# Kernel optimization log

Measured on AMD Instinct MI355X. Metric: run time of the kernel, lower is better.

## Reference

```python
import jax, jax.numpy as jnp
import numpy as np

H = 8        # num_heads
KNN = 16     # k nearest neighbors
D = 256      # input_dim
LN_EPS = 1e-5


def _make_params(key, D):
    ks = jax.random.split(key, 10)
    def lin(k, din, dout):
        k1, k2 = jax.random.split(k)
        lim = 1.0 / np.sqrt(din)
        W = jax.random.uniform(k1, (din, dout), jnp.float32, -lim, lim)
        b = jax.random.uniform(k2, (dout,), jnp.float32, -lim, lim)
        return W, b
    Wq, bq = lin(ks[0], D, D)
    Wk, bk = lin(ks[1], D, D)
    Wv, bv = lin(ks[2], D, D)
    Wo1, bo1 = lin(ks[3], D, D)
    ln_g = jnp.ones((D,), jnp.float32)
    ln_b = jnp.zeros((D,), jnp.float32)
    Wo2, bo2 = lin(ks[4], D, D)
    return dict(Wq=Wq, bq=bq, Wk=Wk, bk=bk, Wv=Wv, bv=bv,
                Wo1=Wo1, bo1=bo1, ln_g=ln_g, ln_b=ln_b, Wo2=Wo2, bo2=bo2)


def setup_inputs() -> dict:
    key = jax.random.key(0)
    k1, k2, k3, k4, k5 = jax.random.split(key, 5)
    B, N, M = 2, 2048, 4096
    inp = {
        "src": jax.random.normal(k1, (B, N, 3), jnp.float32),
        "tgt": jax.random.normal(k2, (B, M, 3), jnp.float32),
        "src_fea": jax.random.normal(k3, (B, N, D), jnp.float32),
        "tgt_fea": jax.random.normal(k4, (B, M, D), jnp.float32),
    }
    inp.update(_make_params(k5, D))
    return inp


def _cdist(x, y):
    # Euclidean distance [B,N,M], matching torch.cdist(p=2)
    x2 = jnp.sum(x * x, axis=-1, keepdims=True)          # [B,N,1]
    y2 = jnp.sum(y * y, axis=-1, keepdims=True)          # [B,M,1]
    sq = x2 + jnp.swapaxes(y2, -1, -2) - 2.0 * jnp.einsum('bnc,bmc->bnm', x, y)
    return jnp.sqrt(jnp.maximum(sq, 0.0))


def _layernorm(x, g, b):
    mu = jnp.mean(x, axis=-1, keepdims=True)
    var = jnp.mean((x - mu) ** 2, axis=-1, keepdims=True)
    return (x - mu) * jax.lax.rsqrt(var + LN_EPS) * g + b


def reference(src, tgt, src_fea, tgt_fea, Wq, bq, Wk, bk, Wv, bv,
              Wo1, bo1, ln_g, ln_b, Wo2, bo2):
    B, N, Dm = src_fea.shape
    M = tgt.shape[1]
    dk = Dm // H
    scale = dk ** (-0.5)

    # kNN mask: distances [B,N,M], topk smallest -> boolean mask
    dist = _cdist(src, tgt)
    _, knn_idx = jax.lax.top_k(-dist, KNN)               # [B,N,KNN]
    bi = jnp.arange(B)[:, None, None]
    ni = jnp.arange(N)[None, :, None]
    mask = jnp.zeros((B, N, M), bool).at[bi, ni, knn_idx].set(True)

    # projections -> [B,H,*,dk]
    Q = (src_fea @ Wq + bq).reshape(B, N, H, dk).transpose(0, 2, 1, 3)
    K = (tgt_fea @ Wk + bk).reshape(B, M, H, dk).transpose(0, 2, 1, 3)
    V = (tgt_fea @ Wv + bv).reshape(B, M, H, dk).transpose(0, 2, 1, 3)

    scores = jnp.einsum('bhnd,bhmd->bhnm', Q, K) * scale
    scores = jnp.where(mask[:, None], scores, -jnp.inf)
    attn = jax.nn.softmax(scores, axis=-1)               # [B,H,N,M]

    out = jnp.einsum('bhnm,bhmd->bhnd', attn, V)
    out = out.transpose(0, 2, 1, 3).reshape(B, N, Dm)

    x = out + src_fea
    h = jax.nn.relu(_layernorm(x @ Wo1 + bo1, ln_g, ln_b))
    updated = h @ Wo2 + bo2

    avg_attn = jnp.mean(attn, axis=1)                    # [B,N,M]
    return updated, avg_attn
```

## Files before the change

kernel.cpp:

```cpp
#include <hip/hip_runtime.h>
#include <math.h>

#define BB 2
#define NN 2048
#define MM 4096
#define DD 256
#define HH 8
#define DK 32
#define KNN 16

typedef __attribute__((ext_vector_type(8))) short short8;
typedef __attribute__((ext_vector_type(4))) short short4v;
typedef __attribute__((ext_vector_type(4))) float f32x4;
typedef unsigned long long u64;
typedef unsigned short u16;

static __device__ __forceinline__ u16 f2bf(float f) {
    union { float f; unsigned u; } v; v.f = f;
    unsigned r = v.u + 0x7FFF + ((v.u >> 16) & 1);
    return (u16)(r >> 16);
}
static __device__ __forceinline__ float bf2f(u16 u) {
    union { unsigned u; float f; } v; v.u = ((unsigned)u) << 16;
    return v.f;
}

__global__ __launch_bounds__(256)
void wtrans(const float* W0, const float* W1, const float* W2, const float* W3, const float* W4,
            u16* O0, u16* O1, u16* O2, u16* O3, u16* O4)
{
    __shared__ float tile[64][65];
    const int bid = blockIdx.x;
    const int m = bid >> 4, tl = bid & 15;
    const int tr = (tl >> 2) * 64, tc = (tl & 3) * 64;
    const float* W = m == 0 ? W0 : m == 1 ? W1 : m == 2 ? W2 : m == 3 ? W3 : W4;
    u16*        O = m == 0 ? O0 : m == 1 ? O1 : m == 2 ? O2 : m == 3 ? O3 : O4;
    const int c = threadIdx.x & 63, r4 = threadIdx.x >> 6;
    #pragma unroll
    for (int i = 0; i < 16; ++i) {
        const int r = (r4 << 4) + i;
        tile[r][c] = W[(size_t)(tr + r) * 256 + tc + c];
    }
    __syncthreads();
    #pragma unroll
    for (int i = 0; i < 16; ++i) {
        const int cc = (r4 << 4) + i;
        O[(size_t)(tc + cc) * 256 + tr + c] = f2bf(tile[c][cc]);
    }
}

static __device__ __forceinline__ void gemm64_body(
    const float* __restrict__ A, size_t row0, const u16* __restrict__ WT, int col0,
    u16* As, u16* Bs, int t, f32x4 acc[2][2])
{
    const int lane = t & 63, w = t >> 6;
    const int wr = (w >> 1) * 32, wc = (w & 1) * 32;
    for (int k0 = 0; k0 < 256; k0 += 64) {
        #pragma unroll
        for (int e = 0; e < 2; ++e) {
            const int flat = t + (e << 8);
            const int r = flat >> 3, kc = (flat & 7) << 3;
            const int off = ((r << 7) + (kc << 1)) ^ ((r & 7) << 4);
            const float* ap = A + (row0 + r) * 256 + k0 + kc;
            float4 a0 = *(const float4*)ap;
            float4 a1 = *(const float4*)(ap + 4);
            short8 s;
            s[0] = (short)f2bf(a0.x); s[1] = (short)f2bf(a0.y);
            s[2] = (short)f2bf(a0.z); s[3] = (short)f2bf(a0.w);
            s[4] = (short)f2bf(a1.x); s[5] = (short)f2bf(a1.y);
            s[6] = (short)f2bf(a1.z); s[7] = (short)f2bf(a1.w);
            *(short8*)((char*)As + off) = s;
            *(short8*)((char*)Bs + off) = *(const short8*)(WT + (size_t)(col0 + r) * 256 + k0 + kc);
        }
        __syncthreads();
        #pragma unroll
        for (int kk = 0; kk < 64; kk += 32) {
            const int kbo = (kk + ((lane >> 4) << 3)) << 1;
            short8 af[2], bfr[2];
            #pragma unroll
            for (int i = 0; i < 2; ++i) {
                const int ra = wr + (i << 4) + (lane & 15);
                af[i]  = *(const short8*)((const char*)As + (((ra << 7) + kbo) ^ ((ra & 7) << 4)));
                const int rb = wc + (i << 4) + (lane & 15);
                bfr[i] = *(const short8*)((const char*)Bs + (((rb << 7) + kbo) ^ ((rb & 7) << 4)));
            }
            #pragma unroll
            for (int mi = 0; mi < 2; ++mi)
                #pragma unroll
                for (int ni = 0; ni < 2; ++ni)
                    acc[mi][ni] = __builtin_amdgcn_mfma_f32_16x16x32_bf16(af[mi], bfr[ni], acc[mi][ni], 0, 0, 0);
        }
        __syncthreads();
    }
}

__global__ __launch_bounds__(256, 4)
void mega_kernel(const float* __restrict__ src, const float* __restrict__ tgt,
                 int* __restrict__ knn_idx,
                 const float* __restrict__ tgt_fea, const float* __restrict__ src_fea,
                 const u16* __restrict__ WTq, const u16* __restrict__ WTkv,
                 const float* __restrict__ bq, const float* __restrict__ bk,
                 const float* __restrict__ bv,
                 float* __restrict__ Qb, u16* __restrict__ Kbf, u16* __restrict__ Vbf,
                 float* __restrict__ avg)
{
    __shared__ u16 As[64 * 64];
    __shared__ u16 Bs[64 * 64];
    const int bid = blockIdx.x;
    const int t = threadIdx.x;
    const int lane = t & 63;
    const int lid = bid / 11;
    const int role = bid % 11;

    if (role < 4) {
        const int kb = lid * 4 + role;
        const int bn = (kb << 2) + (t >> 6);
        const int b = bn >> 11;
        const float* sp = src + (size_t)bn * 3;
        const float px = sp[0], py = sp[1], pz = sp[2];
        const float x2 = px * px + py * py + pz * pz;
        const float* tb = tgt + (size_t)b * MM * 3;
        unsigned key[64];
        #pragma unroll
        for (int j = 0; j < 64; ++j) {
            const int m = (j << 6) + lane;
            const float tx = tb[m * 3 + 0], ty = tb[m * 3 + 1], tz = tb[m * 3 + 2];
            const float y2 = tx * tx + ty * ty + tz * tz;
            const float dt = px * tx + py * ty + pz * tz;
            float d = (x2 + y2) - 2.0f * dt;
            d = d > 0.f ? d : 0.f;
            const unsigned q20 = (unsigned)fminf(d * 32768.0f, 1048575.0f);
            key[j] = (q20 << 12) | (unsigned)m;
        }
        unsigned last1 = 0;
        unsigned mykey = 0xFFFFFFFFu;
        for (int sel = 0; sel < 20; ++sel) {
            unsigned c0 = ~0u, c1 = ~0u, c2 = ~0u, c3 = ~0u;
            #pragma unroll
            for (int j = 0; j < 64; j += 4) {
                const unsigned u0 = key[j + 0] - last1; c0 = u0 < c0 ? u0 : c0;
                const unsigned u1 = key[j + 1] - last1; c1 = u1 < c1 ? u1 : c1;
                const unsigned u2 = key[j + 2] - last1; c2 = u2 < c2 ? u2 : c2;
                const unsigned u3 = key[j + 3] - last1; c3 = u3 < c3 ? u3 : c3;
            }
            unsigned best = c0 < c1 ? c0 : c1;
            const unsigned bst2 = c2 < c3 ? c2 : c3;
            best = best < bst2 ? best : bst2;
            #pragma unroll
            for (int s2 = 32; s2; s2 >>= 1) {
                const unsigned o = __shfl_xor(best, s2, 64);
                best = o < best ? o : best;
            }
            const unsigned winner = best + last1;
            if (lane == sel) mykey = winner;
            last1 = winner + 1;
        }
        const int midx = (int)(mykey & 0xFFFu);
        u64 ex = ~0ULL;
        if (lane < 20) {
            const float* tp = tb + (size_t)midx * 3;
            const double pxd = px, pyd = py, pzd = pz;
            const double tx = tp[0], ty = tp[1], tz = tp[2];
            const double x2d = pxd * pxd + pyd * pyd + pzd * pzd;
            const double y2d = tx * tx + ty * ty + tz * tz;
            const double dtd = pxd * tx + pyd * ty + pzd * tz;
            double dd = (x2d + y2d) - 2.0 * dtd;
            dd = dd > 0.0 ? dd : 0.0;
            ex = (((u64)__double_as_longlong(dd)) & ~0xFFFULL) | (u64)midx;
        }
        int rank = 0;
        #pragma unroll
        for (int i = 0; i < 20; ++i) {
            const u64 o = __shfl(ex, i, 64);
            rank += (o < ex) ? 1 : 0;
        }
        if (lane < 20 && rank < 16)
            knn_idx[(size_t)bn * KNN + rank] = midx;
        return;
    }

    if (role < 8) {
        const int kvb = lid * 4 + (role - 4);
        const size_t row0 = (size_t)(kvb >> 3) * 64;
        const int col0 = (kvb & 7) * 64;
        f32x4 acc[2][2] = {};
        gemm64_body(tgt_fea, row0, WTkv, col0, As, Bs, t, acc);
        const int w = t >> 6;
        const int wr = (w >> 1) * 32, wc = (w & 1) * 32;
        const bool isv = col0 >= 256;
        u16* ob = isv ? Vbf : Kbf;
        const float* bs = isv ? bv : bk;
        const int cb = (isv ? col0 - 256 : col0) + wc;
        const int cq = lane & 15, rq = (lane >> 4) << 2;
        #pragma unroll
        for (int ni = 0; ni < 2; ++ni) {
            const int c = cb + (ni << 4) + cq;
            const float bval = bs[c];
            #pragma unroll
            for (int mi = 0; mi < 2; ++mi) {
                const size_t r = row0 + wr + (mi << 4) + rq;
                #pragma unroll
                for (int e = 0; e < 4; ++e)
                    ob[(r + e) * 256 + c] = f2bf(acc[mi][ni][e] + bval);
            }
        }
        return;
    }

    if (role == 8) {
        const int qb = lid;
        const size_t row0 = (size_t)(qb >> 2) * 64;
        const int col0 = (qb & 3) * 64;
        f32x4 acc[2][2] = {};
        gemm64_body(src_fea, row0, WTq, col0, As, Bs, t, acc);
        const int w = t >> 6;
        const int wr = (w >> 1) * 32, wc = (w & 1) * 32;
        const int cq = lane & 15, rq = (lane >> 4) << 2;
        #pragma unroll
        for (int ni = 0; ni < 2; ++ni) {
            const int c = col0 + wc + (ni << 4) + cq;
            const float bval = bq[c];
            #pragma unroll
            for (int mi = 0; mi < 2; ++mi) {
                const size_t rbase = (row0 + wr + (mi << 4) + rq) * 256 + c;
                #pragma unroll
                for (int e = 0; e < 4; ++e)
                    Qb[rbase + (size_t)e * 256] = acc[mi][ni][e] + bval;
            }
        }
        return;
    }

    {
        const int zb = lid * 2 + (role - 9);
        f32x4 z = {0.f, 0.f, 0.f, 0.f};
        f32x4* pz = (f32x4*)avg;
        const int base = zb * 256 + t;
        #pragma unroll
        for (int i = 0; i < 32; ++i)
            pz[base + i * 131072] = z;
    }
}

__global__ __launch_bounds__(256)
void tail_kernel(const float* __restrict__ Q, const u16* __restrict__ Kb,
                 const u16* __restrict__ Vb, const int* __restrict__ knn_idx,
                 const float* __restrict__ src_fea,
                 const u16* __restrict__ WTo1, const float* __restrict__ bo1,
                 const float* __restrict__ lng, const float* __restrict__ lnb,
                 const u16* __restrict__ WTo2, const float* __restrict__ bo2,
                 float* __restrict__ updated, float* __restrict__ avg_attn)
{
    __shared__ float q_sh[4][256];
    __shared__ float pw_sh[4][8][17];
    __shared__ int   idx_sh[4][16];
    __shared__ u16   Xs[16 * 256];
    __shared__ u16   Hs[16 * 256];
    __shared__ float2 red2[4][4];
    const int t = threadIdx.x;
    const int w = t >> 6, lane = t & 63;
    const int r0 = blockIdx.x << 2;
    const int bn = r0 + w;
    const int b = bn >> 11;
    const int h = lane >> 3, k2 = lane & 7;

    {
        unsigned* xz = (unsigned*)Xs;
        unsigned* hz = (unsigned*)Hs;
        #pragma unroll
        for (int i = 0; i < 6; ++i) {
            xz[512 + t + i * 256] = 0u;
            hz[512 + t + i * 256] = 0u;
        }
    }

    *(float4*)&q_sh[w][lane << 2] = *(const float4*)(Q + (size_t)bn * 256 + (lane << 2));
    const int ia = knn_idx[(size_t)bn * KNN + k2];
    const int ib = knn_idx[(size_t)bn * KNN + 8 + k2];

    const u16* Ka = Kb + ((size_t)b * MM + ia) * 256 + h * DK;
    const u16* Kc = Kb + ((size_t)b * MM + ib) * 256 + h * DK;
    const float* qh = &q_sh[w][h * DK];
    float s0 = 0.f, s1 = 0.f;
    #pragma unroll
    for (int j = 0; j < DK; j += 8) {
        const short8 ka = *(const short8*)(Ka + j);
        const short8 kc = *(const short8*)(Kc + j);
        #pragma unroll
        for (int e = 0; e < 8; ++e) {
            const float qv = qh[j + e];
            s0 = fmaf(qv, bf2f((u16)ka[e]), s0);
            s1 = fmaf(qv, bf2f((u16)kc[e]), s1);
        }
    }
    s0 *= 0.17677669529663688f;
    s1 *= 0.17677669529663688f;

    float mx = fmaxf(s0, s1);
    mx = fmaxf(mx, __shfl_xor(mx, 1, 64));
    mx = fmaxf(mx, __shfl_xor(mx, 2, 64));
    mx = fmaxf(mx, __shfl_xor(mx, 4, 64));
    const float e0 = expf(s0 - mx), e1 = expf(s1 - mx);
    float sum = e0 + e1;
    sum += __shfl_xor(sum, 1, 64);
    sum += __shfl_xor(sum, 2, 64);
    sum += __shfl_xor(sum, 4, 64);
    const float inv = 1.0f / sum;
    const float p0 = e0 * inv, p1 = e1 * inv;

    float a0 = p0, a1 = p1;
    a0 += __shfl_xor(a0, 8, 64);  a1 += __shfl_xor(a1, 8, 64);
    a0 += __shfl_xor(a0, 16, 64); a1 += __shfl_xor(a1, 16, 64);
    a0 += __shfl_xor(a0, 32, 64); a1 += __shfl_xor(a1, 32, 64);
    if (h == 0) {
        avg_attn[(size_t)bn * MM + ia] = a0 * 0.125f;
        avg_attn[(size_t)bn * MM + ib] = a1 * 0.125f;
        idx_sh[w][k2] = ia;
        idx_sh[w][8 + k2] = ib;
    }
    pw_sh[w][h][k2] = p0;
    pw_sh[w][h][8 + k2] = p1;

    {
        const int d0 = lane << 2;
        const int h2 = lane >> 3;
        float o0 = 0.f, o1 = 0.f, o2 = 0.f, o3 = 0.f;
        #pragma unroll
        for (int k = 0; k < KNN; ++k) {
            const float p = pw_sh[w][h2][k];
            const int ik = idx_sh[w][k];
            const short4v v4 = *(const short4v*)(Vb + ((size_t)b * MM + ik) * 256 + d0);
            o0 = fmaf(p, bf2f((u16)v4[0]), o0);
            o1 = fmaf(p, bf2f((u16)v4[1]), o1);
            o2 = fmaf(p, bf2f((u16)v4[2]), o2);
            o3 = fmaf(p, bf2f((u16)v4[3]), o3);
        }
        const float4 sf = *(const float4*)(src_fea + (size_t)bn * 256 + d0);
        short4v xo;
        xo[0] = (short)f2bf(o0 + sf.x);
        xo[1] = (short)f2bf(o1 + sf.y);
        xo[2] = (short)f2bf(o2 + sf.z);
        xo[3] = (short)f2bf(o3 + sf.w);
        const int off = ((w << 9) + (d0 << 1)) ^ ((w & 7) << 4);
        *(short4v*)((char*)Xs + off) = xo;
    }
    __syncthreads();

    const int cq = lane & 15, ks = lane >> 4;
    f32x4 acc1[4] = {};
    #pragma unroll
    for (int s = 0; s < 4; ++s) {
        const int colB = (w << 6) + (s << 4) + cq;
        const u16* bp = WTo1 + (size_t)colB * 256;
        #pragma unroll
        for (int kk = 0; kk < 256; kk += 32) {
            const int k8 = kk + (ks << 3);
            const short8 af = *(const short8*)((const char*)Xs + (((cq << 9) + (k8 << 1)) ^ ((cq & 7) << 4)));
            const short8 bfrg = *(const short8*)(bp + k8);
            acc1[s] = __builtin_amdgcn_mfma_f32_16x16x32_bf16(af, bfrg, acc1[s], 0, 0, 0);
        }
        const float bval = bo1[colB];
        #pragma unroll
        for (int e = 0; e < 4; ++e) acc1[s][e] += bval;
    }
    {
        #pragma unroll
        for (int e = 0; e < 4; ++e) {
            float v = acc1[0][e] + acc1[1][e] + acc1[2][e] + acc1[3][e];
            float vv = acc1[0][e]*acc1[0][e] + acc1[1][e]*acc1[1][e]
                     + acc1[2][e]*acc1[2][e] + acc1[3][e]*acc1[3][e];
            v += __shfl_xor(v, 1, 64); vv += __shfl_xor(vv, 1, 64);
            v += __shfl_xor(v, 2, 64); vv += __shfl_xor(vv, 2, 64);
            v += __shfl_xor(v, 4, 64); vv += __shfl_xor(vv, 4, 64);
            v += __shfl_xor(v, 8, 64); vv += __shfl_xor(vv, 8, 64);
            if (ks == 0 && cq == 0) {
                float2 pr; pr.x = v; pr.y = vv;
                red2[w][e] = pr;
            }
        }
    }
    __syncthreads();
    if (ks == 0) {
        float g4[4], b4[4];
        #pragma unroll
        for (int s = 0; s < 4; ++s) {
            const int colB = (w << 6) + (s << 4) + cq;
            g4[s] = lng[colB]; b4[s] = lnb[colB];
        }
        #pragma unroll
        for (int e = 0; e < 4; ++e) {
            float S1 = 0.f, S2 = 0.f;
            #pragma unroll
            for (int w2 = 0; w2 < 4; ++w2) {
                const float2 pr = red2[w2][e];
                S1 += pr.x; S2 += pr.y;
            }
            const float mean = S1 * (1.0f / 256.0f);
            const float var = S2 * (1.0f / 256.0f) - mean * mean;
            const float rstd = 1.0f / sqrtf(var + 1e-5f);
            #pragma unroll
            for (int s = 0; s < 4; ++s) {
                const int colB = (w << 6) + (s << 4) + cq;
                const float y = (acc1[s][e] - mean) * rstd * g4[s] + b4[s];
                const int off = ((e << 9) + (colB << 1)) ^ ((e & 7) << 4);
                *(u16*)((char*)Hs + off) = f2bf(fmaxf(y, 0.0f));
            }
        }
    }
    __syncthreads();

    #pragma unroll
    for (int s = 0; s < 4; ++s) {
        const int colB = (w << 6) + (s << 4) + cq;
        const u16* bp = WTo2 + (size_t)colB * 256;
        f32x4 acc2 = {};
        #pragma unroll
        for (int kk = 0; kk < 256; kk += 32) {
            const int k8 = kk + (ks << 3);
            const short8 af = *(const short8*)((const char*)Hs + (((cq << 9) + (k8 << 1)) ^ ((cq & 7) << 4)));
            const short8 bfrg = *(const short8*)(bp + k8);
            acc2 = __builtin_amdgcn_mfma_f32_16x16x32_bf16(af, bfrg, acc2, 0, 0, 0);
        }
        if (ks == 0) {
            const float bval = bo2[colB];
            #pragma unroll
            for (int e = 0; e < 4; ++e)
                updated[(size_t)(r0 + e) * 256 + colB] = acc2[e] + bval;
        }
    }
}

extern "C" void kernel_launch(void* const* d_in, const int* in_sizes, int n_in,
                              void* d_out, int out_size, void* d_ws, size_t ws_size,
                              hipStream_t stream) {
    const float* src     = (const float*)d_in[0];
    const float* tgt     = (const float*)d_in[1];
    const float* src_fea = (const float*)d_in[2];
    const float* tgt_fea = (const float*)d_in[3];
    const float* Wq  = (const float*)d_in[4];   const float* bq  = (const float*)d_in[5];
    const float* Wk  = (const float*)d_in[6];   const float* bk  = (const float*)d_in[7];
    const float* Wv  = (const float*)d_in[8];   const float* bv  = (const float*)d_in[9];
    const float* Wo1 = (const float*)d_in[10];  const float* bo1 = (const float*)d_in[11];
    const float* lng = (const float*)d_in[12];  const float* lnb = (const float*)d_in[13];
    const float* Wo2 = (const float*)d_in[14];  const float* bo2 = (const float*)d_in[15];
    (void)in_sizes; (void)n_in; (void)out_size; (void)ws_size;

    float* out     = (float*)d_out;
    float* updated = out;
    float* avg     = out + (size_t)BB * NN * DD;

    char* p = (char*)d_ws;
    u16* WTq  = (u16*)p;   p += 256 * 256 * 2;
    u16* WTk  = (u16*)p;   p += 256 * 256 * 2;
    u16* WTv  = (u16*)p;   p += 256 * 256 * 2;
    u16* WTo1 = (u16*)p;   p += 256 * 256 * 2;
    u16* WTo2 = (u16*)p;   p += 256 * 256 * 2;
    float* Qb = (float*)p; p += (size_t)BB * NN * DD * 4;
    u16* Kbf  = (u16*)p;   p += (size_t)BB * MM * DD * 2;
    u16* Vbf  = (u16*)p;   p += (size_t)BB * MM * DD * 2;
    int* knn  = (int*)p;   p += (size_t)BB * NN * KNN * 4;

    dim3 blk(256);
    wtrans<<<80, blk, 0, stream>>>(Wq, Wk, Wv, Wo1, Wo2, WTq, WTk, WTv, WTo1, WTo2);
    mega_kernel<<<2816, blk, 0, stream>>>(src, tgt, knn, tgt_fea, src_fea, WTq, WTk,
                                          bq, bk, bv, Qb, Kbf, Vbf, avg);
    tail_kernel<<<1024, blk, 0, stream>>>(Qb, Kbf, Vbf, knn, src_fea,
                                          WTo1, bo1, lng, lnb, WTo2, bo2,
                                          updated, avg);
}
```

Measured before the change: 196.2 us.

## Replace per-lane 64-key register array with streaming top-2 and lazy refill

```diff
diff --git a/kernel.cpp b/kernel.cpp
--- a/kernel.cpp
+++ b/kernel.cpp
@@ -92,6 +92,24 @@
         }
         __syncthreads();
     }
+}
+
+static __device__ __forceinline__ unsigned refill_gt(
+    const float* __restrict__ tb, int lane, float px, float py, float pz,
+    float x2, unsigned lastPop)
+{
+    unsigned best = 0xFFFFFFFFu;
+    #pragma unroll 1
+    for (int j = 0; j < 64; ++j) {
+        const int m = (j << 6) + lane;
+        const float tx = tb[m*3+0], ty = tb[m*3+1], tz = tb[m*3+2];
+        const float y2 = tx*tx + ty*ty + tz*tz;
+        float d = (x2 + y2) - 2.0f*(px*tx + py*ty + pz*tz);
+        d = d > 0.f ? d : 0.f;
+        const unsigned k = ((unsigned)fminf(d * 32768.0f, 1048574.0f) << 12) | (unsigned)m;
+        if (k > lastPop && k < best) best = k;
+    }
+    return best;
 }
 
 __global__ __launch_bounds__(256, 4)
@@ -120,40 +138,38 @@
         const float px = sp[0], py = sp[1], pz = sp[2];
         const float x2 = px * px + py * py + pz * pz;
         const float* tb = tgt + (size_t)b * MM * 3;
-        unsigned key[64];
-        #pragma unroll
+        unsigned s0 = 0xFFFFFFFFu, s1 = 0xFFFFFFFFu;
+        #pragma unroll 8
         for (int j = 0; j < 64; ++j) {
             const int m = (j << 6) + lane;
             const float tx = tb[m * 3 + 0], ty = tb[m * 3 + 1], tz = tb[m * 3 + 2];
             const float y2 = tx * tx + ty * ty + tz * tz;
-            const float dt = px * tx + py * ty + pz * tz;
-            float d = (x2 + y2) - 2.0f * dt;
+            float d = (x2 + y2) - 2.0f * (px * tx + py * ty + pz * tz);
             d = d > 0.f ? d : 0.f;
-            const unsigned q20 = (unsigned)fminf(d * 32768.0f, 1048575.0f);
-            key[j] = (q20 << 12) | (unsigned)m;
-        }
-        unsigned last1 = 0;
-        unsigned mykey = 0xFFFFFFFFu;
+            const unsigned k = ((unsigned)fminf(d * 32768.0f, 1048574.0f) << 12) | (unsigned)m;
+            const unsigned hi = k > s0 ? k : s0;
+            s0 = k < s0 ? k : s0;
+            s1 = hi < s1 ? hi : s1;
+        }
+        unsigned lastPop = 0;
+        unsigned mykey = 0;
         for (int sel = 0; sel < 20; ++sel) {
-            unsigned c0 = ~0u, c1 = ~0u, c2 = ~0u, c3 = ~0u;
-            #pragma unroll
-            for (int j = 0; j < 64; j += 4) {
-                const unsigned u0 = key[j + 0] - last1; c0 = u0 < c0 ? u0 : c0;
-                const unsigned u1 = key[j + 1] - last1; c1 = u1 < c1 ? u1 : c1;
-                const unsigned u2 = key[j + 2] - last1; c2 = u2 < c2 ? u2 : c2;
-                const unsigned u3 = key[j + 3] - last1; c3 = u3 < c3 ? u3 : c3;
-            }
-            unsigned best = c0 < c1 ? c0 : c1;
-            const unsigned bst2 = c2 < c3 ? c2 : c3;
-            best = best < bst2 ? best : bst2;
+            if (__any(s0 == 0xFFFFFFFFu)) {
+                if (s0 == 0xFFFFFFFFu)
+                    s0 = refill_gt(tb, lane, px, py, pz, x2, lastPop);
+            }
+            unsigned best = s0;
             #pragma unroll
             for (int s2 = 32; s2; s2 >>= 1) {
                 const unsigned o = __shfl_xor(best, s2, 64);
                 best = o < best ? o : best;
             }
-            const unsigned winner = best + last1;
-            if (lane == sel) mykey = winner;
-            last1 = winner + 1;
+            if (lane == sel) mykey = best;
+            if (s0 == best) {
+                lastPop = s0;
+                s0 = s1;
+                s1 = 0xFFFFFFFFu;
+            }
         }
         const int midx = (int)(mykey & 0xFFFu);
         u64 ex = ~0ULL;
```

Result: slower. 242.1 us (+23.4%).
